# Optimization experiments

Hardware: AMD Instinct MI355X
Metric: run time of the kernel (lower is better)

The kernel has to match this reference:

```python
import jax, jax.numpy as jnp
import numpy as np

N = 50000   # nodes
E = 1600000 # edges (avg degree 32)
D = 128     # in_feats
H = 128     # n_hidden
C = 47      # n_classes


def setup_inputs() -> dict:
    key = jax.random.key(0)
    ks = jax.random.split(key, 10)
    w = lambda k, i, o: jax.random.normal(k, (i, o), jnp.float32) * 0.05
    return {
        "feat": jax.random.normal(ks[0], (N, D), jnp.float32),
        "src": jax.random.randint(ks[1], (E,), 0, N),
        "dst": jax.random.randint(ks[2], (E,), 0, N),
        "Wself0": w(ks[3], D, H), "Wneigh0": w(ks[4], D, H), "b0": jnp.zeros((H,), jnp.float32),
        "Wself1": w(ks[5], H, H), "Wneigh1": w(ks[6], H, H), "b1": jnp.zeros((H,), jnp.float32),
        "Wfc": w(ks[7], H, C), "bfc": jnp.zeros((C,), jnp.float32),
    }


def _sage_mean(feat, src, dst, Wself, Wneigh, b):
    # gather source features along edges, segment-mean into destination nodes
    msgs = feat[src]                                              # [E, d]
    agg = jax.ops.segment_sum(msgs, dst, num_segments=N)          # [N, d]
    deg = jax.ops.segment_sum(jnp.ones((E,), feat.dtype), dst, num_segments=N)
    h_neigh = agg / jnp.maximum(deg, 1.0)[:, None]                # mean, deg-0 safe
    return feat @ Wself + h_neigh @ Wneigh + b


def reference(feat, src, dst, Wself0, Wneigh0, b0, Wself1, Wneigh1, b1, Wfc, bfc):
    h = jax.nn.relu(_sage_mean(feat, src, dst, Wself0, Wneigh0, b0))
    h = jax.nn.relu(_sage_mean(h, src, dst, Wself1, Wneigh1, b1))
    return h @ Wfc + bfc
```

## Files before the change

### kernel.cpp

```cpp
#include <hip/hip_runtime.h>

#define NN 50000
#define NE 1600000
#define NBA 200
#define CPB (NE / NBA)
#define NBUCK 196
#define MAXBE 12288

typedef unsigned int uint;
typedef __attribute__((ext_vector_type(8))) short short8;
typedef __attribute__((ext_vector_type(4))) float f32x4;
typedef __attribute__((ext_vector_type(4), aligned(4))) float f32x4u;


__device__ __forceinline__ uint bf16rne(float f) {
  uint u = __float_as_uint(f);
  return (u + 0x7fffu + ((u >> 16) & 1u)) >> 16;
}
__device__ __forceinline__ uint packbf2(float lo, float hi) {
  return bf16rne(lo) | (bf16rne(hi) << 16);
}
__device__ __forceinline__ float bflo(uint u) { return __uint_as_float(u << 16); }
__device__ __forceinline__ float bfhi(uint u) { return __uint_as_float(u & 0xffff0000u); }

__device__ __forceinline__ short8 as_short8(uint4 v) {
  union { uint4 u; short8 s; } cv; cv.u = v; return cv.s;
}

__device__ __forceinline__ void add8(const uint4 v, float* a) {
  a[0] += bflo(v.x); a[1] += bfhi(v.x);
  a[2] += bflo(v.y); a[3] += bfhi(v.y);
  a[4] += bflo(v.z); a[5] += bfhi(v.z);
  a[6] += bflo(v.w); a[7] += bfhi(v.w);
}

__global__ __launch_bounds__(256) void tobf16_kernel(const float* __restrict__ in,
                                                     uint* __restrict__ outb, int n8) {
  int t = blockIdx.x * 256 + threadIdx.x;
  if (t < n8) {
    float4 a = ((const float4*)in)[2 * t];
    float4 b = ((const float4*)in)[2 * t + 1];
    uint4 o;
    o.x = packbf2(a.x, a.y);
    o.y = packbf2(a.z, a.w);
    o.z = packbf2(b.x, b.y);
    o.w = packbf2(b.z, b.w);
    ((uint4*)outb)[t] = o;
  }
}


__global__ __launch_bounds__(256) void packW_kernel(const float* __restrict__ W00,
                                                    const float* __restrict__ W01,
                                                    const float* __restrict__ W10,
                                                    const float* __restrict__ W11,
                                                    const float* __restrict__ Wfc,
                                                    uint4* __restrict__ Wpack) {
  int t = blockIdx.x * 256 + threadIdx.x;
  if (t < 16384) {
    int lane = t & 63;
    int ks   = (t >> 6) & 3;
    int ft   = (t >> 8) & 7;
    int part = (t >> 11) & 1;
    int mat  = (t >> 12) & 1;
    int layer= (t >> 13) & 1;
    const float* Wsrc = layer ? (mat ? W11 : W10) : (mat ? W01 : W00);
    int feat  = ft * 16 + (lane & 15);
    int kbase = ks * 32 + (lane >> 4) * 8;
    uint o[4];
#pragma unroll
    for (int h = 0; h < 4; ++h) {
      float w0 = Wsrc[(kbase + 2 * h) * 128 + feat];
      float w1 = Wsrc[(kbase + 2 * h + 1) * 128 + feat];
      uint h0 = bf16rne(w0), h1 = bf16rne(w1);
      uint v0, v1;
      if (part == 0) { v0 = h0; v1 = h1; }
      else {
        v0 = bf16rne(w0 - __uint_as_float(h0 << 16));
        v1 = bf16rne(w1 - __uint_as_float(h1 << 16));
      }
      o[h] = v0 | (v1 << 16);
    }
    uint4 r; r.x = o[0]; r.y = o[1]; r.z = o[2]; r.w = o[3];
    Wpack[t] = r;
  } else if (t < 16384 + 1536) {
    int tt = t - 16384;
    int lane = tt & 63;
    int ks   = (tt >> 6) & 3;
    int ct   = (tt >> 8) % 3;
    int part = tt / 768;
    int col  = ct * 16 + (lane & 15);
    int kbase = ks * 32 + (lane >> 4) * 8;
    uint o[4];
#pragma unroll
    for (int h = 0; h < 4; ++h) {
      float w0 = (col < 47) ? Wfc[(kbase + 2 * h) * 47 + col] : 0.f;
      float w1 = (col < 47) ? Wfc[(kbase + 2 * h + 1) * 47 + col] : 0.f;
      uint h0 = bf16rne(w0), h1 = bf16rne(w1);
      uint v0, v1;
      if (part == 0) { v0 = h0; v1 = h1; }
      else {
        v0 = bf16rne(w0 - __uint_as_float(h0 << 16));
        v1 = bf16rne(w1 - __uint_as_float(h1 << 16));
      }
      o[h] = v0 | (v1 << 16);
    }
    uint4 r; r.x = o[0]; r.y = o[1]; r.z = o[2]; r.w = o[3];
    Wpack[t] = r;
  }
}


__global__ __launch_bounds__(1024) void histA_kernel(const int* __restrict__ dst,
                                                     int* __restrict__ histA) {
  __shared__ int h[NBUCK];
  int tid = threadIdx.x, b = blockIdx.x;
  if (tid < NBUCK) h[tid] = 0;
  __syncthreads();
  const int4* d4 = (const int4*)(dst + b * CPB);
  for (int i = tid; i < CPB / 4; i += 1024) {
    int4 d = d4[i];
    atomicAdd(&h[d.x >> 8], 1);
    atomicAdd(&h[d.y >> 8], 1);
    atomicAdd(&h[d.z >> 8], 1);
    atomicAdd(&h[d.w >> 8], 1);
  }
  __syncthreads();
  if (tid < NBUCK) histA[b * NBUCK + tid] = h[tid];
}

__global__ __launch_bounds__(256) void scanA_kernel(int* __restrict__ histA,
                                                    int* __restrict__ bucket_base) {
  __shared__ int wsum[4];
  int t = threadIdx.x;
  int s = 0;
  if (t < NBUCK) {
#pragma unroll 8
    for (int b = 0; b < NBA; ++b) {
      int v = histA[b * NBUCK + t];
      histA[b * NBUCK + t] = s;
      s += v;
    }
  }
  int lane = t & 63, wid = t >> 6;
  int x = s;
#pragma unroll
  for (int d = 1; d < 64; d <<= 1) {
    int y = __shfl_up(x, d, 64);
    if (lane >= d) x += y;
  }
  if (lane == 63) wsum[wid] = x;
  __syncthreads();
  int woff = 0;
  if (wid > 0) woff += wsum[0];
  if (wid > 1) woff += wsum[1];
  if (wid > 2) woff += wsum[2];
  int excl = woff + x - s;
  if (t < NBUCK) bucket_base[t] = excl;
  if (t == NBUCK - 1) bucket_base[NBUCK] = excl + s;
}

__global__ __launch_bounds__(1024) void scatterA_kernel(const int* __restrict__ src,
                                                        const int* __restrict__ dst,
                                                        const int* __restrict__ histA,
                                                        const int* __restrict__ bucket_base,
                                                        uint* __restrict__ gbuf) {
  __shared__ int cur[NBUCK];
  int tid = threadIdx.x, b = blockIdx.x;
  if (tid < NBUCK) cur[tid] = histA[b * NBUCK + tid] + bucket_base[tid];
  __syncthreads();
  const int4* d4 = (const int4*)(dst + b * CPB);
  const int4* s4 = (const int4*)(src + b * CPB);
  for (int i = tid; i < CPB / 4; i += 1024) {
    int4 d = d4[i];
    int4 s = s4[i];
    int p0 = atomicAdd(&cur[d.x >> 8], 1);
    int p1 = atomicAdd(&cur[d.y >> 8], 1);
    int p2 = atomicAdd(&cur[d.z >> 8], 1);
    int p3 = atomicAdd(&cur[d.w >> 8], 1);
    gbuf[p0] = (uint)s.x | ((uint)(d.x & 255) << 16);
    gbuf[p1] = (uint)s.y | ((uint)(d.y & 255) << 16);
    gbuf[p2] = (uint)s.z | ((uint)(d.z & 255) << 16);
    gbuf[p3] = (uint)s.w | ((uint)(d.w & 255) << 16);
  }
}

__global__ __launch_bounds__(1024) void passB_kernel(const uint* __restrict__ gbuf,
                                                     const int* __restrict__ bucket_base,
                                                     int* __restrict__ offs,
                                                     int* __restrict__ csr) {
  __shared__ int cnt_l[256];
  __shared__ int cur_l[256];
  __shared__ int wsum[4];
  int tid = threadIdx.x, b = blockIdx.x;
  int bbase = bucket_base[b];
  int nE = bucket_base[b + 1] - bbase;
  int lo = b << 8;
  if (tid < 256) cnt_l[tid] = 0;
  __syncthreads();

  const uint* gptr = gbuf + bbase;
  uint pv[MAXBE / 1024];
#pragma unroll
  for (int j = 0; j < MAXBE / 1024; ++j) {
    int i = tid + j * 1024;
    if (i < nE) {
      uint p = gptr[i];
      pv[j] = p;
      atomicAdd(&cnt_l[(p >> 16) & 255], 1);
    }
  }
  __syncthreads();

  int excl = 0, v = 0;
  if (tid < 256) {
    v = cnt_l[tid];
    int lane = tid & 63, wid = tid >> 6;
    int x = v;
#pragma unroll
    for (int d = 1; d < 64; d <<= 1) {
      int y = __shfl_up(x, d, 64);
      if (lane >= d) x += y;
    }
    if (lane == 63) wsum[wid] = x;
    __syncthreads();
    int woff = 0;
    if (wid > 0) woff += wsum[0];
    if (wid > 1) woff += wsum[1];
    if (wid > 2) woff += wsum[2];
    excl = woff + x - v;
    cur_l[tid] = excl;
    int node = lo + tid;
    if (node <= NN) offs[node] = bbase + excl;
  } else {
    __syncthreads();
  }
  __syncthreads();

#pragma unroll
  for (int j = 0; j < MAXBE / 1024; ++j) {
    int i = tid + j * 1024;
    if (i < nE) {
      uint p = pv[j];
      int r = atomicAdd(&cur_l[(p >> 16) & 255], 1);
      csr[bbase + r] = (int)(p & 0xFFFFu);
    }
  }
}


__global__ __launch_bounds__(256) void agg_kernel(const uint* __restrict__ Xb,
                                                  const int* __restrict__ csr,
                                                  const int* __restrict__ offs,
                                                  uint* __restrict__ outb, int N) {
  const uint4* __restrict__ X4 = (const uint4*)Xb;
  int tid = threadIdx.x;
  int slot = tid >> 4;
  int lane = tid & 15;
  int n = blockIdx.x * 16 + slot;
  if (n >= N) return;
  int s = offs[n], e = offs[n + 1];

  float aA[8] = {0.f, 0.f, 0.f, 0.f, 0.f, 0.f, 0.f, 0.f};
  float aB[8] = {0.f, 0.f, 0.f, 0.f, 0.f, 0.f, 0.f, 0.f};

  int j = s;
  for (; j + 8 <= e; j += 8) {
    int i0 = csr[j + 0], i1 = csr[j + 1], i2 = csr[j + 2], i3 = csr[j + 3];
    int i4 = csr[j + 4], i5 = csr[j + 5], i6 = csr[j + 6], i7 = csr[j + 7];
    uint4 v0 = X4[i0 * 16 + lane];
    uint4 v1 = X4[i1 * 16 + lane];
    uint4 v2 = X4[i2 * 16 + lane];
    uint4 v3 = X4[i3 * 16 + lane];
    uint4 v4 = X4[i4 * 16 + lane];
    uint4 v5 = X4[i5 * 16 + lane];
    uint4 v6 = X4[i6 * 16 + lane];
    uint4 v7 = X4[i7 * 16 + lane];
    add8(v0, aA); add8(v1, aA); add8(v2, aA); add8(v3, aA);
    add8(v4, aB); add8(v5, aB); add8(v6, aB); add8(v7, aB);
  }
  for (; j < e; ++j) {
    uint4 v = X4[csr[j] * 16 + lane];
    add8(v, aA);
  }

  float inv = 1.0f / fmaxf((float)(e - s), 1.0f);
  uint4 o;
  o.x = packbf2((aA[0] + aB[0]) * inv, (aA[1] + aB[1]) * inv);
  o.y = packbf2((aA[2] + aB[2]) * inv, (aA[3] + aB[3]) * inv);
  o.z = packbf2((aA[4] + aB[4]) * inv, (aA[5] + aB[5]) * inv);
  o.w = packbf2((aA[6] + aB[6]) * inv, (aA[7] + aB[7]) * inv);
  ((uint4*)outb)[n * 16 + lane] = o;
}


#define MFMA16(a, b, c) __builtin_amdgcn_mfma_f32_16x16x32_bf16((a), (b), (c), 0, 0, 0)

__global__ __launch_bounds__(512) void gemm_mfma(
    const uint* __restrict__ As_g, const uint* __restrict__ An_g,
    const uint4* __restrict__ Wp,
    const float* __restrict__ bias, uint* __restrict__ Out,
    const uint4* __restrict__ Wfcp, const float* __restrict__ bfc,
    float* __restrict__ OutFC, int do_fc, int N) {
  __shared__ uint4 sT[2][16][17];
  __shared__ uint4 h2s[128][17];
  int tid = threadIdx.x;
  int lane = tid & 63;
  int ft = tid >> 6;
  int ng = blockIdx.x;
  int l15 = lane & 15, lhi = lane >> 4;

  short8 aH[2][4], aL[2][4];
#pragma unroll
  for (int m = 0; m < 2; ++m)
#pragma unroll
    for (int ks = 0; ks < 4; ++ks) {
      aH[m][ks] = as_short8(Wp[(m * 2 + 0) * 2048 + ft * 256 + ks * 64 + lane]);
      aL[m][ks] = as_short8(Wp[(m * 2 + 1) * 2048 + ft * 256 + ks * 64 + lane]);
    }
  int feat0 = ft * 16 + lhi * 4;
  float bv0 = bias[feat0], bv1 = bias[feat0 + 1];
  float bv2 = bias[feat0 + 2], bv3 = bias[feat0 + 3];

  const uint4* __restrict__ Xs = (const uint4*)As_g;
  const uint4* __restrict__ Xn = (const uint4*)An_g;

  int smat = tid >> 8;
  int sidx = tid & 255;
  int srow = sidx >> 4;
  int scol = sidx & 15;

  for (int t = 0; t < 8; ++t) {
    int grow = ng * 128 + t * 16 + srow;
    if (grow >= N) grow = N - 1;
    const uint4* srcp = smat ? Xn : Xs;
    sT[smat][srow][scol] = srcp[grow * 16 + scol];
    __syncthreads();

    f32x4 acc = {0.f, 0.f, 0.f, 0.f};
    short8 b;
#pragma unroll
    for (int ks = 0; ks < 4; ++ks) {
      b = as_short8(sT[0][l15][ks * 4 + lhi]);
      acc = MFMA16(aH[0][ks], b, acc);
      acc = MFMA16(aL[0][ks], b, acc);
    }
#pragma unroll
    for (int ks = 0; ks < 4; ++ks) {
      b = as_short8(sT[1][l15][ks * 4 + lhi]);
      acc = MFMA16(aH[1][ks], b, acc);
      acc = MFMA16(aL[1][ks], b, acc);
    }

    int rloc = t * 16 + l15;
    int row = ng * 128 + rloc;
    float o0 = fmaxf(acc[0] + bv0, 0.f);
    float o1 = fmaxf(acc[1] + bv1, 0.f);
    float o2 = fmaxf(acc[2] + bv2, 0.f);
    float o3 = fmaxf(acc[3] + bv3, 0.f);
    uint2 st;
    st.x = packbf2(o0, o1);
    st.y = packbf2(o2, o3);
    if (do_fc) {
      ((uint2*)&h2s[rloc][0])[ft * 4 + lhi] = st;
    } else if (row < N) {
      ((uint2*)Out)[row * 32 + ft * 4 + lhi] = st;
    }
    __syncthreads();
  }

  if (do_fc) {
    short8 fH[3][4], fL[3][4];
#pragma unroll
    for (int ct = 0; ct < 3; ++ct)
#pragma unroll
      for (int ks = 0; ks < 4; ++ks) {
        fH[ct][ks] = as_short8(Wfcp[((0 * 3 + ct) * 4 + ks) * 64 + lane]);
        fL[ct][ks] = as_short8(Wfcp[((1 * 3 + ct) * 4 + ks) * 64 + lane]);
      }
    int rloc = ft * 16 + l15;
    int row = ng * 128 + rloc;
    short8 v0 = as_short8(h2s[rloc][0 * 4 + lhi]);
    short8 v1 = as_short8(h2s[rloc][1 * 4 + lhi]);
    short8 v2 = as_short8(h2s[rloc][2 * 4 + lhi]);
    short8 v3 = as_short8(h2s[rloc][3 * 4 + lhi]);

    f32x4 facc[3];
#pragma unroll
    for (int ct = 0; ct < 3; ++ct) {
      f32x4 a = {0.f, 0.f, 0.f, 0.f};
      a = MFMA16(fH[ct][0], v0, a); a = MFMA16(fL[ct][0], v0, a);
      a = MFMA16(fH[ct][1], v1, a); a = MFMA16(fL[ct][1], v1, a);
      a = MFMA16(fH[ct][2], v2, a); a = MFMA16(fL[ct][2], v2, a);
      a = MFMA16(fH[ct][3], v3, a); a = MFMA16(fL[ct][3], v3, a);
      facc[ct] = a;
    }

    if (row < N) {
      float* orow = OutFC + (size_t)row * 47;
#pragma unroll
      for (int ct = 0; ct < 3; ++ct) {
        int col0 = ct * 16 + lhi * 4;
        if (col0 + 3 < 47) {
          f32x4u stv;
          stv[0] = facc[ct][0] + bfc[col0];
          stv[1] = facc[ct][1] + bfc[col0 + 1];
          stv[2] = facc[ct][2] + bfc[col0 + 2];
          stv[3] = facc[ct][3] + bfc[col0 + 3];
          *(f32x4u*)(orow + col0) = stv;
        } else {
#pragma unroll
          for (int r = 0; r < 4; ++r) {
            int col = col0 + r;
            if (col < 47) orow[col] = facc[ct][r] + bfc[col];
          }
        }
      }
    }
  }
}


extern "C" void kernel_launch(void* const* d_in, const int* in_sizes, int n_in,
                              void* d_out, int out_size, void* d_ws, size_t ws_size,
                              hipStream_t stream) {
  const float* feat    = (const float*)d_in[0];
  const int*   src     = (const int*)d_in[1];
  const int*   dst     = (const int*)d_in[2];
  const float* Wself0  = (const float*)d_in[3];
  const float* Wneigh0 = (const float*)d_in[4];
  const float* b0      = (const float*)d_in[5];
  const float* Wself1  = (const float*)d_in[6];
  const float* Wneigh1 = (const float*)d_in[7];
  const float* b1      = (const float*)d_in[8];
  const float* Wfc     = (const float*)d_in[9];
  const float* bfc     = (const float*)d_in[10];
  float* out = (float*)d_out;

  char* w = (char*)d_ws;
  int*   offs    = (int*)(w);
  int*   bbase   = (int*)(w + 262144);
  int*   histA   = (int*)(w + 266240);
  int*   csr     = (int*)(w + 524288);
  uint4* Wpack   = (uint4*)(w + 7340032);
  uint*  featb   = (uint*)(w + 7864320);
  uint*  gbuf    = (uint*)(w + 20971520);
  uint*  hnb     = (uint*)(w + 27787264);
  uint*  h0b     = (uint*)(w + 41943040);

  const int N = NN;

  histA_kernel<<<NBA, 1024, 0, stream>>>(dst, histA);
  scanA_kernel<<<1, 256, 0, stream>>>(histA, bbase);
  scatterA_kernel<<<NBA, 1024, 0, stream>>>(src, dst, histA, bbase, gbuf);
  passB_kernel<<<NBUCK, 1024, 0, stream>>>(gbuf, bbase, offs, csr);

  tobf16_kernel<<<(N * 16 + 255) / 256, 256, 0, stream>>>(feat, featb, N * 16);
  packW_kernel<<<70, 256, 0, stream>>>(Wself0, Wneigh0, Wself1, Wneigh1, Wfc, Wpack);

  const int gblocks = (N + 127) / 128;

  agg_kernel<<<(N + 15) / 16, 256, 0, stream>>>(featb, csr, offs, hnb, N);
  gemm_mfma<<<gblocks, 512, 0, stream>>>(featb, hnb, Wpack, b0, h0b,
                                         Wpack + 16384, bfc, out, 0, N);
  agg_kernel<<<(N + 15) / 16, 256, 0, stream>>>(h0b, csr, offs, hnb, N);
  gemm_mfma<<<gblocks, 512, 0, stream>>>(h0b, hnb, Wpack + 8192, b1, h0b,
                                         Wpack + 16384, bfc, out, 1, N);
}
```

Before: 183.0 us.

## Fuse histogram, bf16 conversion and weight packing into one prep kernel; transpose histogram

Merges the per-chunk dst histogram, the feature fp32-to-bf16 conversion and the weight packing into a single launch that dispatches on block index, so the three independent jobs run concurrently and two launches disappear. The histogram is also stored transposed (bucket-major), which lets the single-block scan read each bucket's row with contiguous int4 loads instead of strided scalar loads. In exchange, scatterA now reads the histogram with a strided pattern, and the fused kernel uses 1024-thread blocks for all three roles.

```diff
diff --git a/kernel.cpp b/kernel.cpp
--- a/kernel.cpp
+++ b/kernel.cpp
@@ -6,6 +6,8 @@
 #define CPB (NE / NBA)
 #define NBUCK 196
 #define MAXBE 12288
+#define TB_BLOCKS 782
+#define PW_BLOCKS 18
 
 typedef unsigned int uint;
 typedef __attribute__((ext_vector_type(8))) short short8;
@@ -34,112 +36,114 @@
   a[6] += bflo(v.w); a[7] += bfhi(v.w);
 }
 
-__global__ __launch_bounds__(256) void tobf16_kernel(const float* __restrict__ in,
-                                                     uint* __restrict__ outb, int n8) {
-  int t = blockIdx.x * 256 + threadIdx.x;
-  if (t < n8) {
-    float4 a = ((const float4*)in)[2 * t];
-    float4 b = ((const float4*)in)[2 * t + 1];
-    uint4 o;
-    o.x = packbf2(a.x, a.y);
-    o.y = packbf2(a.z, a.w);
-    o.z = packbf2(b.x, b.y);
-    o.w = packbf2(b.z, b.w);
-    ((uint4*)outb)[t] = o;
-  }
-}
-
-
-__global__ __launch_bounds__(256) void packW_kernel(const float* __restrict__ W00,
-                                                    const float* __restrict__ W01,
-                                                    const float* __restrict__ W10,
-                                                    const float* __restrict__ W11,
-                                                    const float* __restrict__ Wfc,
-                                                    uint4* __restrict__ Wpack) {
-  int t = blockIdx.x * 256 + threadIdx.x;
-  if (t < 16384) {
-    int lane = t & 63;
-    int ks   = (t >> 6) & 3;
-    int ft   = (t >> 8) & 7;
-    int part = (t >> 11) & 1;
-    int mat  = (t >> 12) & 1;
-    int layer= (t >> 13) & 1;
-    const float* Wsrc = layer ? (mat ? W11 : W10) : (mat ? W01 : W00);
-    int feat  = ft * 16 + (lane & 15);
-    int kbase = ks * 32 + (lane >> 4) * 8;
-    uint o[4];
-#pragma unroll
-    for (int h = 0; h < 4; ++h) {
-      float w0 = Wsrc[(kbase + 2 * h) * 128 + feat];
-      float w1 = Wsrc[(kbase + 2 * h + 1) * 128 + feat];
-      uint h0 = bf16rne(w0), h1 = bf16rne(w1);
-      uint v0, v1;
-      if (part == 0) { v0 = h0; v1 = h1; }
-      else {
-        v0 = bf16rne(w0 - __uint_as_float(h0 << 16));
-        v1 = bf16rne(w1 - __uint_as_float(h1 << 16));
+
+__global__ __launch_bounds__(1024) void prep_kernel(
+    const int* __restrict__ dst, int* __restrict__ histAT,
+    const float* __restrict__ feat, uint* __restrict__ featb,
+    const float* __restrict__ W00, const float* __restrict__ W01,
+    const float* __restrict__ W10, const float* __restrict__ W11,
+    const float* __restrict__ Wfc, uint4* __restrict__ Wpack) {
+  __shared__ int h[NBUCK];
+  int tid = threadIdx.x, bid = blockIdx.x;
+
+  if (bid < NBA) {
+    if (tid < NBUCK) h[tid] = 0;
+    __syncthreads();
+    const int4* d4 = (const int4*)(dst + bid * CPB);
+    for (int i = tid; i < CPB / 4; i += 1024) {
+      int4 d = d4[i];
+      atomicAdd(&h[d.x >> 8], 1);
+      atomicAdd(&h[d.y >> 8], 1);
+      atomicAdd(&h[d.z >> 8], 1);
+      atomicAdd(&h[d.w >> 8], 1);
+    }
+    __syncthreads();
+    if (tid < NBUCK) histAT[tid * NBA + bid] = h[tid];
+  } else if (bid < NBA + TB_BLOCKS) {
+    int t = (bid - NBA) * 1024 + tid;
+    if (t < NN * 16) {
+      float4 a = ((const float4*)feat)[2 * t];
+      float4 b = ((const float4*)feat)[2 * t + 1];
+      uint4 o;
+      o.x = packbf2(a.x, a.y);
+      o.y = packbf2(a.z, a.w);
+      o.z = packbf2(b.x, b.y);
+      o.w = packbf2(b.z, b.w);
+      ((uint4*)featb)[t] = o;
+    }
+  } else {
+    int t = (bid - NBA - TB_BLOCKS) * 1024 + tid;
+    if (t < 16384) {
+      int lane = t & 63;
+      int ks   = (t >> 6) & 3;
+      int ft   = (t >> 8) & 7;
+      int part = (t >> 11) & 1;
+      int mat  = (t >> 12) & 1;
+      int layer= (t >> 13) & 1;
+      const float* Wsrc = layer ? (mat ? W11 : W10) : (mat ? W01 : W00);
+      int feat_i = ft * 16 + (lane & 15);
+      int kbase = ks * 32 + (lane >> 4) * 8;
+      uint o[4];
+#pragma unroll
+      for (int hh = 0; hh < 4; ++hh) {
+        float w0 = Wsrc[(kbase + 2 * hh) * 128 + feat_i];
+        float w1 = Wsrc[(kbase + 2 * hh + 1) * 128 + feat_i];
+        uint h0 = bf16rne(w0), h1 = bf16rne(w1);
+        uint v0, v1;
+        if (part == 0) { v0 = h0; v1 = h1; }
+        else {
+          v0 = bf16rne(w0 - __uint_as_float(h0 << 16));
+          v1 = bf16rne(w1 - __uint_as_float(h1 << 16));
+        }
+        o[hh] = v0 | (v1 << 16);
       }
-      o[h] = v0 | (v1 << 16);
-    }
-    uint4 r; r.x = o[0]; r.y = o[1]; r.z = o[2]; r.w = o[3];
-    Wpack[t] = r;
-  } else if (t < 16384 + 1536) {
-    int tt = t - 16384;
-    int lane = tt & 63;
-    int ks   = (tt >> 6) & 3;
-    int ct   = (tt >> 8) % 3;
-    int part = tt / 768;
-    int col  = ct * 16 + (lane & 15);
-    int kbase = ks * 32 + (lane >> 4) * 8;
-    uint o[4];
-#pragma unroll
-    for (int h = 0; h < 4; ++h) {
-      float w0 = (col < 47) ? Wfc[(kbase + 2 * h) * 47 + col] : 0.f;
-      float w1 = (col < 47) ? Wfc[(kbase + 2 * h + 1) * 47 + col] : 0.f;
-      uint h0 = bf16rne(w0), h1 = bf16rne(w1);
-      uint v0, v1;
-      if (part == 0) { v0 = h0; v1 = h1; }
-      else {
-        v0 = bf16rne(w0 - __uint_as_float(h0 << 16));
-        v1 = bf16rne(w1 - __uint_as_float(h1 << 16));
+      uint4 r; r.x = o[0]; r.y = o[1]; r.z = o[2]; r.w = o[3];
+      Wpack[t] = r;
+    } else if (t < 16384 + 1536) {
+      int tt = t - 16384;
+      int lane = tt & 63;
+      int ks   = (tt >> 6) & 3;
+      int ct   = (tt >> 8) % 3;
+      int part = tt / 768;
+      int col  = ct * 16 + (lane & 15);
+      int kbase = ks * 32 + (lane >> 4) * 8;
+      uint o[4];
+#pragma unroll
+      for (int hh = 0; hh < 4; ++hh) {
+        float w0 = (col < 47) ? Wfc[(kbase + 2 * hh) * 47 + col] : 0.f;
+        float w1 = (col < 47) ? Wfc[(kbase + 2 * hh + 1) * 47 + col] : 0.f;
+        uint h0 = bf16rne(w0), h1 = bf16rne(w1);
+        uint v0, v1;
+        if (part == 0) { v0 = h0; v1 = h1; }
+        else {
+          v0 = bf16rne(w0 - __uint_as_float(h0 << 16));
+          v1 = bf16rne(w1 - __uint_as_float(h1 << 16));
+        }
+        o[hh] = v0 | (v1 << 16);
       }
-      o[h] = v0 | (v1 << 16);
-    }
-    uint4 r; r.x = o[0]; r.y = o[1]; r.z = o[2]; r.w = o[3];
-    Wpack[t] = r;
-  }
-}
-
-
-__global__ __launch_bounds__(1024) void histA_kernel(const int* __restrict__ dst,
-                                                     int* __restrict__ histA) {
-  __shared__ int h[NBUCK];
-  int tid = threadIdx.x, b = blockIdx.x;
-  if (tid < NBUCK) h[tid] = 0;
-  __syncthreads();
-  const int4* d4 = (const int4*)(dst + b * CPB);
-  for (int i = tid; i < CPB / 4; i += 1024) {
-    int4 d = d4[i];
-    atomicAdd(&h[d.x >> 8], 1);
-    atomicAdd(&h[d.y >> 8], 1);
-    atomicAdd(&h[d.z >> 8], 1);
-    atomicAdd(&h[d.w >> 8], 1);
-  }
-  __syncthreads();
-  if (tid < NBUCK) histA[b * NBUCK + tid] = h[tid];
-}
-
-__global__ __launch_bounds__(256) void scanA_kernel(int* __restrict__ histA,
+      uint4 r; r.x = o[0]; r.y = o[1]; r.z = o[2]; r.w = o[3];
+      Wpack[t] = r;
+    }
+  }
+}
+
+
+__global__ __launch_bounds__(256) void scanA_kernel(int* __restrict__ histAT,
                                                     int* __restrict__ bucket_base) {
   __shared__ int wsum[4];
   int t = threadIdx.x;
   int s = 0;
   if (t < NBUCK) {
-#pragma unroll 8
-    for (int b = 0; b < NBA; ++b) {
-      int v = histA[b * NBUCK + t];
-      histA[b * NBUCK + t] = s;
-      s += v;
+    int4* row = (int4*)(histAT + t * NBA);
+#pragma unroll 10
+    for (int b4 = 0; b4 < NBA / 4; ++b4) {
+      int4 v = row[b4];
+      int4 w;
+      w.x = s; s += v.x;
+      w.y = s; s += v.y;
+      w.z = s; s += v.z;
+      w.w = s; s += v.w;
+      row[b4] = w;
     }
   }
   int lane = t & 63, wid = t >> 6;
@@ -162,12 +166,12 @@
 
 __global__ __launch_bounds__(1024) void scatterA_kernel(const int* __restrict__ src,
                                                         const int* __restrict__ dst,
-                                                        const int* __restrict__ histA,
+                                                        const int* __restrict__ histAT,
                                                         const int* __restrict__ bucket_base,
                                                         uint* __restrict__ gbuf) {
   __shared__ int cur[NBUCK];
   int tid = threadIdx.x, b = blockIdx.x;
-  if (tid < NBUCK) cur[tid] = histA[b * NBUCK + tid] + bucket_base[tid];
+  if (tid < NBUCK) cur[tid] = histAT[tid * NBA + b] + bucket_base[tid];
   __syncthreads();
   const int4* d4 = (const int4*)(dst + b * CPB);
   const int4* s4 = (const int4*)(src + b * CPB);
@@ -440,7 +444,7 @@
   char* w = (char*)d_ws;
   int*   offs    = (int*)(w);
   int*   bbase   = (int*)(w + 262144);
-  int*   histA   = (int*)(w + 266240);
+  int*   histAT  = (int*)(w + 266240);
   int*   csr     = (int*)(w + 524288);
   uint4* Wpack   = (uint4*)(w + 7340032);
   uint*  featb   = (uint*)(w + 7864320);
@@ -450,13 +454,11 @@
 
   const int N = NN;
 
-  histA_kernel<<<NBA, 1024, 0, stream>>>(dst, histA);
-  scanA_kernel<<<1, 256, 0, stream>>>(histA, bbase);
-  scatterA_kernel<<<NBA, 1024, 0, stream>>>(src, dst, histA, bbase, gbuf);
+  prep_kernel<<<NBA + TB_BLOCKS + PW_BLOCKS, 1024, 0, stream>>>(
+      dst, histAT, feat, featb, Wself0, Wneigh0, Wself1, Wneigh1, Wfc, Wpack);
+  scanA_kernel<<<1, 256, 0, stream>>>(histAT, bbase);
+  scatterA_kernel<<<NBA, 1024, 0, stream>>>(src, dst, histAT, bbase, gbuf);
   passB_kernel<<<NBUCK, 1024, 0, stream>>>(gbuf, bbase, offs, csr);
-
-  tobf16_kernel<<<(N * 16 + 255) / 256, 256, 0, stream>>>(feat, featb, N * 16);
-  packW_kernel<<<70, 256, 0, stream>>>(Wself0, Wneigh0, Wself1, Wneigh1, Wfc, Wpack);
 
   const int gblocks = (N + 127) / 128;
 
```

New measurement: 179.9 us. No clear change (-1.7%).
